# Kernel tuning notes

Hardware: AMD Instinct MI355X
Metric: run time of the kernel (lower is better)

## Reference

```python
import math
import jax, jax.numpy as jnp
import numpy as np

HEAD_DIM = 128
NUM_HEADS = 16
NUM_KV_HEADS = 4
CAUSAL = True


def rotate_half(x):
    x1 = x[..., : x.shape[-1] // 2]
    x2 = x[..., x.shape[-1] // 2 :]
    return jnp.concatenate([-x2, x1], axis=-1)


def setup_inputs() -> dict:
    key = jax.random.key(0)
    k1, k2, k3, k4, k5 = jax.random.split(key, 5)
    B, S, H = 2, 2048, 2048
    total_heads = NUM_HEADS + 2 * NUM_KV_HEADS  # 24
    hidden_states = jax.random.normal(k1, (B, S, H), dtype=jnp.float32)
    cos = jax.random.normal(k2, (S, HEAD_DIM), dtype=jnp.float32)
    sin = jax.random.normal(k3, (S, HEAD_DIM), dtype=jnp.float32)
    # eqx.nn.Linear weight layout: [out_features, in_features], y = W @ x
    w_qkv = jax.random.normal(k4, (total_heads * HEAD_DIM, H), dtype=jnp.float32) / math.sqrt(H)
    w_o = jax.random.normal(k5, (H, NUM_HEADS * HEAD_DIM), dtype=jnp.float32) / math.sqrt(NUM_HEADS * HEAD_DIM)
    return {"hidden_states": hidden_states, "cos": cos, "sin": sin, "w_qkv": w_qkv, "w_o": w_o}


def reference(hidden_states, cos, sin, w_qkv, w_o):
    B, S, _ = hidden_states.shape
    # fused QKV projection: [B,S,total_heads,head_dim]
    qkv = jnp.einsum("bsh,oh->bso", hidden_states, w_qkv).reshape(B, S, -1, HEAD_DIM)
    q = qkv[:, :, :NUM_HEADS]
    k = qkv[:, :, NUM_HEADS : NUM_HEADS + NUM_KV_HEADS]
    v = qkv[:, :, NUM_HEADS + NUM_KV_HEADS :]
    # RoPE: cos/sin [S,head_dim] -> broadcast [S,1,head_dim] over heads
    c = cos[..., None, :]
    s_ = sin[..., None, :]
    q = q * c + rotate_half(q) * s_
    k = k * c + rotate_half(k) * s_
    # GQA: repeat K/V across query-head groups
    rep = NUM_HEADS // NUM_KV_HEADS
    k = jnp.repeat(k, rep, axis=2)
    v = jnp.repeat(v, rep, axis=2)
    scale = 1.0 / math.sqrt(HEAD_DIM)
    scores = jnp.einsum("bshd,bthd->bhst", q, k) * scale  # [B,H,S,S]
    if CAUSAL:
        mask = jnp.tril(jnp.ones((S, S), dtype=bool))[None, None]
        scores = jnp.where(mask, scores, jnp.float32(-1e10))
    attn = jax.nn.softmax(scores, axis=-1)
    out = jnp.einsum("bhst,bthd->bshd", attn, v).reshape(B, S, -1)
    return jnp.einsum("bsd,od->bso", out, w_o)
```

## Files before the change

kernel.cpp:

```cpp
#include <hip/hip_runtime.h>
#include <hip/hip_bf16.h>
#include <stdint.h>

typedef __hip_bfloat16 bf16;
typedef __attribute__((ext_vector_type(8))) __bf16 bf16x8;
typedef __attribute__((ext_vector_type(4))) float f32x4;
typedef __attribute__((ext_vector_type(16))) float f32x16;
typedef __attribute__((ext_vector_type(4))) unsigned int u32x4;

#define QSCALE_LOG2E (0.08838834764831845f * 1.4426950408889634f)

__device__ __forceinline__ float fast_exp2(float x) {
#if __has_builtin(__builtin_amdgcn_exp2f)
  return __builtin_amdgcn_exp2f(x);
#else
  return exp2f(x);
#endif
}

__device__ __forceinline__ void gload_lds16(const void* g, void* l) {
  __builtin_amdgcn_global_load_lds(
      (__attribute__((address_space(1))) void*)(uintptr_t)g,
      (__attribute__((address_space(3))) void*)(uint32_t)(uintptr_t)l,
      16, 0, 0);
}

__global__ void cast_f32_to_bf16(const float* __restrict__ in,
                                 bf16* __restrict__ out, int n) {
  const int n4 = n >> 2;
  const int stride = gridDim.x * blockDim.x;
  for (int i = blockIdx.x * blockDim.x + threadIdx.x; i < n4; i += stride) {
    float4 v = reinterpret_cast<const float4*>(in)[i];
    bf16 tmp[4];
    tmp[0] = __float2bfloat16(v.x);
    tmp[1] = __float2bfloat16(v.y);
    tmp[2] = __float2bfloat16(v.z);
    tmp[3] = __float2bfloat16(v.w);
    reinterpret_cast<uint2*>(out)[i] = *reinterpret_cast<uint2*>(tmp);
  }
}

__device__ __forceinline__ void store_c(float v, bf16* p) { *p = __float2bfloat16(v); }
__device__ __forceinline__ void store_c(float v, float* p) { *p = v; }

__device__ __forceinline__ bf16x8 rd_swz(const bf16* base, int row, int ks, int hi) {
  const int byte = row * 128 + ((ks * 64 + hi * 16) ^ ((row & 7) << 4));
  return *reinterpret_cast<const bf16x8*>((const char*)base + byte);
}

__device__ __forceinline__ void stage_part(const bf16* __restrict__ g, int K,
                                           int kt, bf16* ldsBase, int part,
                                           int tid) {
  const int ga = part * 512 + tid;
  const int r = ga >> 3;
  const int gl = ga & 7;
  const int col = kt * 64 + ((gl ^ (r & 7)) << 3);
  gload_lds16(g + (size_t)r * K + col, (char*)ldsBase + ga * 16);
}

#define DS_A(QR)                                                              \
  _Pragma("unroll") for (int m = 0; m < 4; ++m)                               \
  _Pragma("unroll") for (int ks = 0; ks < 2; ++ks)                            \
      af[m][ks] = rd_swz(Acur, wm * 128 + (QR) * 64 + m * 16 + lr, ks, hi);

#define DS_B0()                                                               \
  _Pragma("unroll") for (int n = 0; n < NQ0; ++n)                             \
  _Pragma("unroll") for (int ks = 0; ks < 2; ++ks)                            \
      bf0[n][ks] = rd_swz(Bcur, wn * WN + n * 16 + lr, ks, hi);

#define DS_B1()                                                               \
  _Pragma("unroll") for (int n = 0; n < NQ1; ++n)                             \
  _Pragma("unroll") for (int ks = 0; ks < 2; ++ks)                            \
      bf1[n][ks] = rd_swz(Bcur, wn * WN + (NQ0 + n) * 16 + lr, ks, hi);

#define MFMA_Q0(QR)                                                           \
  __builtin_amdgcn_s_setprio(1);                                             \
  _Pragma("unroll") for (int ks = 0; ks < 2; ++ks)                            \
  _Pragma("unroll") for (int m = 0; m < 4; ++m)                               \
  _Pragma("unroll") for (int n = 0; n < NQ0; ++n)                             \
      acc[(QR) * 4 + m][n] = __builtin_amdgcn_mfma_f32_16x16x32_bf16(         \
          af[m][ks], bf0[n][ks], acc[(QR) * 4 + m][n], 0, 0, 0);              \
  __builtin_amdgcn_s_setprio(0);

#define MFMA_Q1(QR)                                                           \
  __builtin_amdgcn_s_setprio(1);                                             \
  _Pragma("unroll") for (int ks = 0; ks < 2; ++ks)                            \
  _Pragma("unroll") for (int m = 0; m < 4; ++m)                               \
  _Pragma("unroll") for (int n = 0; n < NQ1; ++n)                             \
      acc[(QR) * 4 + m][NQ0 + n] = __builtin_amdgcn_mfma_f32_16x16x32_bf16(   \
          af[m][ks], bf1[n][ks], acc[(QR) * 4 + m][NQ0 + n], 0, 0, 0);        \
  __builtin_amdgcn_s_setprio(0);

#define PHASE_SYNC_PRE()                                \
  __builtin_amdgcn_s_barrier();                         \
  asm volatile("s_waitcnt lgkmcnt(0)" ::: "memory");    \
  __builtin_amdgcn_sched_barrier(0);

#define PHASE_END() __builtin_amdgcn_s_barrier();

#define VMCNT_LB()                                                            \
  if constexpr (LB == 2) asm volatile("s_waitcnt vmcnt(2)" ::: "memory");     \
  else if constexpr (LB == 3) asm volatile("s_waitcnt vmcnt(3)" ::: "memory");\
  else asm volatile("s_waitcnt vmcnt(4)" ::: "memory");

template <int BN, typename OutT>
__global__ __launch_bounds__(512, 2) void gemm256(const bf16* __restrict__ A,
                                                  const bf16* __restrict__ B,
                                                  OutT* __restrict__ C,
                                                  int M, int N, int K, int NBX) {
  constexpr int NFRAG = BN / 64;
  constexpr int NQ0 = (NFRAG + 1) / 2;
  constexpr int NQ1 = NFRAG - NQ0;
  constexpr int WN = BN / 4;
  constexpr int LB = BN / 64;
  constexpr int LB0 = (LB + 1) / 2;
  constexpr int LB1 = LB - LB0;

  extern __shared__ bf16 sm[];
  bf16* A0 = sm;
  bf16* A1 = sm + 16384;
  bf16* B0 = sm + 32768;
  bf16* B1 = B0 + BN * 64;

  const int tid = threadIdx.x;
  const int lane = tid & 63;
  const int w = tid >> 6;
  const int wm = w >> 2;
  const int wn = w & 3;
  const int lr = lane & 15;
  const int hi = lane >> 4;

  const int nwg = gridDim.x;
  const int cpx = nwg >> 3;
  const int bid = blockIdx.x;
  const int wg = (bid & 7) * cpx + (bid >> 3);
  const int bx = wg % NBX;
  const int by = wg / NBX;
  const int row0 = by * 256;
  const int col0 = bx * BN;

  const bf16* Ag = A + (size_t)row0 * K;
  const bf16* Bg = B + (size_t)col0 * K;

#pragma unroll
  for (int p = 0; p < 4; ++p) stage_part(Ag, K, 0, A0, p, tid);
#pragma unroll
  for (int p = 0; p < LB; ++p) stage_part(Bg, K, 0, B0, p, tid);
#pragma unroll
  for (int p = 0; p < LB; ++p) stage_part(Bg, K, 1, B1, p, tid);
  VMCNT_LB();
  __builtin_amdgcn_s_barrier();

  f32x4 acc[8][NFRAG] = {};
  bf16x8 af[4][2], bf0[NQ0][2], bf1[NQ1 ? NQ1 : 1][2];

  const int iters = K >> 7;
  for (int i = 0; i < iters; ++i) {
    const bool g2 = (i + 1 < iters);
    const int t1 = 2 * i + 1, t2 = 2 * i + 2, t3 = 2 * i + 3;
    {
      const bf16* Acur = A0;
      const bf16* Bcur = B0;
      DS_A(0); DS_B0();
      stage_part(Ag, K, t1, A1, 0, tid);
      stage_part(Ag, K, t1, A1, 1, tid);
      PHASE_SYNC_PRE(); MFMA_Q0(0); PHASE_END();
      DS_B1();
      stage_part(Ag, K, t1, A1, 2, tid);
      stage_part(Ag, K, t1, A1, 3, tid);
      PHASE_SYNC_PRE(); MFMA_Q1(0); PHASE_END();
      DS_A(1);
      if (g2) {
#pragma unroll
        for (int p = 0; p < LB0; ++p) stage_part(Bg, K, t2, B0, p, tid);
      }
      PHASE_SYNC_PRE(); MFMA_Q0(1); PHASE_END();
      if (g2) {
#pragma unroll
        for (int p = 0; p < LB1; ++p) stage_part(Bg, K, t2, B0, LB0 + p, tid);
        VMCNT_LB();
      } else {
        asm volatile("s_waitcnt vmcnt(0)" ::: "memory");
      }
      PHASE_SYNC_PRE(); MFMA_Q1(1); PHASE_END();
    }
    {
      const bf16* Acur = A1;
      const bf16* Bcur = B1;
      DS_A(0); DS_B0();
      if (g2) {
        stage_part(Ag, K, t2, A0, 0, tid);
        stage_part(Ag, K, t2, A0, 1, tid);
      }
      PHASE_SYNC_PRE(); MFMA_Q0(0); PHASE_END();
      DS_B1();
      if (g2) {
        stage_part(Ag, K, t2, A0, 2, tid);
        stage_part(Ag, K, t2, A0, 3, tid);
      }
      PHASE_SYNC_PRE(); MFMA_Q1(0); PHASE_END();
      DS_A(1);
      if (g2) {
#pragma unroll
        for (int p = 0; p < LB0; ++p) stage_part(Bg, K, t3, B1, p, tid);
      }
      PHASE_SYNC_PRE(); MFMA_Q0(1); PHASE_END();
      if (g2) {
#pragma unroll
        for (int p = 0; p < LB1; ++p) stage_part(Bg, K, t3, B1, LB0 + p, tid);
        VMCNT_LB();
      } else {
        asm volatile("s_waitcnt vmcnt(0)" ::: "memory");
      }
      PHASE_SYNC_PRE(); MFMA_Q1(1); PHASE_END();
    }
  }

#pragma unroll
  for (int mi = 0; mi < 8; ++mi)
#pragma unroll
    for (int ni = 0; ni < NFRAG; ++ni)
#pragma unroll
      for (int j = 0; j < 4; ++j) {
        const int r = row0 + wm * 128 + mi * 16 + hi * 4 + j;
        const int cc = col0 + wn * WN + ni * 16 + lr;
        store_c(acc[mi][ni][j], &C[(size_t)r * N + cc]);
      }
}

__global__ void rope_scatter(const bf16* __restrict__ qkv,
                             const float* __restrict__ cs,
                             const float* __restrict__ sn,
                             bf16* __restrict__ Q, bf16* __restrict__ Kd) {
  const int tok = blockIdx.x;
  const int b = tok >> 11;
  const int s = tok & 2047;
  const bf16* row = qkv + (size_t)tok * 3072;
  for (int idx = threadIdx.x; idx < 1280; idx += blockDim.x) {
    const int head = idx >> 6;
    const int j = idx & 63;
    float x1 = __bfloat162float(row[head * 128 + j]);
    float x2 = __bfloat162float(row[head * 128 + j + 64]);
    const float c1 = cs[s * 128 + j];
    const float c2 = cs[s * 128 + j + 64];
    const float s1 = sn[s * 128 + j];
    const float s2 = sn[s * 128 + j + 64];
    float y1 = x1 * c1 - x2 * s1;
    float y2 = x2 * c2 + x1 * s2;
    bf16* dst;
    if (head < 16) {
      y1 *= QSCALE_LOG2E;
      y2 *= QSCALE_LOG2E;
      dst = Q + ((size_t)(b * 16 + head) * 2048 + s) * 128;
    } else {
      dst = Kd + ((size_t)(b * 4 + head - 16) * 2048 + s) * 128;
    }
    dst[j] = __float2bfloat16(y1);
    dst[j + 64] = __float2bfloat16(y2);
  }
}

__global__ __launch_bounds__(256) void vtrans(const bf16* __restrict__ qkv,
                                              bf16* __restrict__ Vt) {
  __shared__ bf16 tile[64 * 136];
  const int bid = blockIdx.x;
  const int stile = bid & 31;
  const int hv = (bid >> 5) & 3;
  const int b = bid >> 7;
  const int tid = threadIdx.x;
  const int tok0 = stile * 64;
  const bf16* src = qkv + (size_t)(b * 2048 + tok0) * 3072 + 2560 + hv * 128;
#pragma unroll
  for (int i = 0; i < 4; ++i) {
    const int c = tid + i * 256;
    const int r = c >> 4;
    const int off = (c & 15) * 8;
    uint4 d = *reinterpret_cast<const uint4*>(src + (size_t)r * 3072 + off);
    *reinterpret_cast<uint4*>(&tile[r * 136 + off]) = d;
  }
  __syncthreads();
  bf16* dst = Vt + ((size_t)(b * 4 + hv) * 128) * 2048 + tok0;
#pragma unroll
  for (int i = 0; i < 4; ++i) {
    const int o = tid + i * 256;
    const int d = o >> 3;
    const int s0 = (o & 7) * 8;
    bf16 vals[8];
#pragma unroll
    for (int j = 0; j < 8; ++j) vals[j] = tile[(s0 + j) * 136 + d];
    *reinterpret_cast<uint4*>(dst + (size_t)d * 2048 + s0) =
        *reinterpret_cast<const uint4*>(vals);
  }
}

__device__ __forceinline__ void stage_k(const bf16* __restrict__ Kb, int k0,
                                        bf16* dst, int w, int lane) {
#pragma unroll
  for (int i = 0; i < 4; ++i) {
    const int L16 = i * 256 + w * 64 + lane;
    const int row = L16 >> 4;
    const int colb = (L16 & 15) * 16;
    const int src = colb ^ ((row & 7) << 4);
    gload_lds16(Kb + (size_t)(k0 + row) * 128 + (src >> 1),
                (char*)dst + (i * 256 + w * 64) * 16);
  }
}

__device__ __forceinline__ void stage_v(const bf16* __restrict__ Vtb, int k0,
                                        bf16* dst, int w, int lane) {
#pragma unroll
  for (int i = 0; i < 4; ++i) {
    const int L16 = i * 256 + w * 64 + lane;
    const int row = L16 >> 3;
    const int colb = (L16 & 7) * 16;
    const int src = colb ^ ((row & 7) << 4);
    gload_lds16(Vtb + (size_t)row * 2048 + k0 + (src >> 1),
                (char*)dst + (i * 256 + w * 64) * 16);
  }
}

__device__ __forceinline__ bf16x8 lds_read_swz(const bf16* base, int row,
                                               int colElem, int rowBytes) {
  const int byte = row * rowBytes + (((colElem * 2) ^ ((row & 7) << 4)));
  return *reinterpret_cast<const bf16x8*>((const char*)base + byte);
}

__global__ __launch_bounds__(256, 2) void attn_fwd(const bf16* __restrict__ Qg,
                                                   const bf16* __restrict__ Kg,
                                                   const bf16* __restrict__ Vtg,
                                                   bf16* __restrict__ Og) {
  __shared__ bf16 Ks[2][64 * 128];
  __shared__ bf16 Vs[2][128 * 64];

  const int tid = threadIdx.x;
  const int lane = tid & 63;
  const int w = tid >> 6;
  const int bid = blockIdx.x;
  int qt, bh;
  if (bid < 256) { qt = bid & 15; bh = bid >> 4; }
  else           { qt = 15 - (bid & 15); bh = 16 + ((bid - 256) >> 4); }
  const int b = bh >> 4;
  const int h = bh & 15;
  const int kvh = h >> 2;
  const int q31 = lane & 31;
  const int hw = lane >> 5;

  const bf16* Qb = Qg + ((size_t)(b * 16 + h) * 2048) * 128;
  const bf16* Kb = Kg + ((size_t)(b * 4 + kvh) * 2048) * 128;
  const bf16* Vtb = Vtg + ((size_t)(b * 4 + kvh) * 128) * 2048;

  const int qw = qt * 128 + w * 32;

  bf16x8 qf[8];
#pragma unroll
  for (int db = 0; db < 8; ++db)
    qf[db] = *reinterpret_cast<const bf16x8*>(Qb + (size_t)(qw + q31) * 128 +
                                              db * 16 + hw * 8);

  f32x16 acc[4] = {};
  float mrow = -1e30f;
  float lsum = 0.f;

  const int nt = 2 * qt + 2;

  stage_k(Kb, 0, &Ks[0][0], w, lane);
  stage_v(Vtb, 0, &Vs[0][0], w, lane);

  for (int t = 0; t < nt; ++t) {
    const int cur = t & 1;
    if (t + 1 < nt) {
      stage_k(Kb, (t + 1) * 64, &Ks[cur ^ 1][0], w, lane);
      stage_v(Vtb, (t + 1) * 64, &Vs[cur ^ 1][0], w, lane);
      asm volatile("s_waitcnt vmcnt(8)" ::: "memory");
    } else {
      asm volatile("s_waitcnt vmcnt(0)" ::: "memory");
    }
    __builtin_amdgcn_s_barrier();
    __builtin_amdgcn_sched_barrier(0);

    const int k0 = t * 64;
    const bool active = (k0 <= qw + 31);
    if (active) {
      const bf16* Kt = &Ks[cur][0];
      const bf16* Vtl = &Vs[cur][0];

      f32x16 sacc[2] = {};
#pragma unroll
      for (int kb = 0; kb < 2; ++kb)
#pragma unroll
        for (int db = 0; db < 8; ++db) {
          bf16x8 kf = lds_read_swz(Kt, kb * 32 + q31, db * 16 + hw * 8, 256);
          sacc[kb] = __builtin_amdgcn_mfma_f32_32x32x16_bf16(kf, qf[db],
                                                             sacc[kb], 0, 0, 0);
        }

      float p[2][16];
#pragma unroll
      for (int kb = 0; kb < 2; ++kb)
#pragma unroll
        for (int r = 0; r < 16; ++r) p[kb][r] = sacc[kb][r];

      if (k0 + 63 > qw) {
        const int qg = qw + q31;
#pragma unroll
        for (int kb = 0; kb < 2; ++kb)
#pragma unroll
          for (int r = 0; r < 16; ++r) {
            const int k = k0 + kb * 32 + (r & 3) + 8 * (r >> 2) + 4 * hw;
            if (k > qg) p[kb][r] = -1e30f;
          }
      }

      float mt = p[0][0];
#pragma unroll
      for (int r = 1; r < 16; ++r) mt = fmaxf(mt, p[0][r]);
#pragma unroll
      for (int r = 0; r < 16; ++r) mt = fmaxf(mt, p[1][r]);
      mt = fmaxf(mt, __shfl_xor(mt, 32));

      if (__any(mt > mrow + 11.5f)) {
        const float mnew = fmaxf(mrow, mt);
        const float alpha = fast_exp2(mrow - mnew);
        mrow = mnew;
        lsum *= alpha;
        float areg[16];
#pragma unroll
        for (int r = 0; r < 16; ++r) {
          const int qloc = (r & 3) + 8 * (r >> 2) + 4 * hw;
          areg[r] = __shfl(alpha, qloc + (lane & 32));
        }
#pragma unroll
        for (int db = 0; db < 4; ++db)
#pragma unroll
          for (int r = 0; r < 16; ++r) acc[db][r] *= areg[r];
      }

      float rs = 0.f;
#pragma unroll
      for (int kb = 0; kb < 2; ++kb)
#pragma unroll
        for (int r = 0; r < 16; ++r) {
          const float pe = fast_exp2(p[kb][r] - mrow);
          p[kb][r] = pe;
          rs += pe;
        }
      rs += __shfl_xor(rs, 32);
      lsum += rs;

      unsigned int pk[2][8];
#pragma unroll
      for (int kb = 0; kb < 2; ++kb)
#pragma unroll
        for (int i = 0; i < 8; ++i)
          asm("v_cvt_pk_bf16_f32 %0, %1, %2"
              : "=v"(pk[kb][i])
              : "v"(p[kb][2 * i]), "v"(p[kb][2 * i + 1]));

#pragma unroll
      for (int kb16 = 0; kb16 < 4; ++kb16) {
        const int kb = kb16 >> 1;
        const int j0 = (kb16 & 1) * 4;
        unsigned int a0 = pk[kb][j0 + 0], b0 = pk[kb][j0 + 2];
        unsigned int a1 = pk[kb][j0 + 1], b1 = pk[kb][j0 + 3];
        asm volatile("v_permlane32_swap_b32 %0, %1" : "+v"(a0), "+v"(b0));
        asm volatile("v_permlane32_swap_b32 %0, %1" : "+v"(a1), "+v"(b1));
        u32x4 afu;
        afu.x = a0; afu.y = a1; afu.z = b0; afu.w = b1;
        bf16x8 pa;
        __builtin_memcpy(&pa, &afu, 16);
#pragma unroll
        for (int db = 0; db < 4; ++db) {
          bf16x8 vf = lds_read_swz(Vtl, db * 32 + q31, kb16 * 16 + hw * 8, 128);
          acc[db] = __builtin_amdgcn_mfma_f32_32x32x16_bf16(pa, vf,
                                                            acc[db], 0, 0, 0);
        }
      }
    }

    __builtin_amdgcn_sched_barrier(0);
    __builtin_amdgcn_s_barrier();
  }

  const float inv = 1.0f / lsum;
  float invq[16];
#pragma unroll
  for (int r = 0; r < 16; ++r) {
    const int qloc = (r & 3) + 8 * (r >> 2) + 4 * hw;
    invq[r] = __shfl(inv, qloc + (lane & 32));
  }
#pragma unroll
  for (int db = 0; db < 4; ++db)
#pragma unroll
    for (int r = 0; r < 16; ++r) {
      const int qg = qw + (r & 3) + 8 * (r >> 2) + 4 * hw;
      const int dg = db * 32 + q31;
      Og[((size_t)(b * 2048 + qg)) * 2048 + h * 128 + dg] =
          __float2bfloat16(acc[db][r] * invq[r]);
    }
}

extern "C" void kernel_launch(void* const* d_in, const int* in_sizes, int n_in,
                              void* d_out, int out_size, void* d_ws,
                              size_t ws_size, hipStream_t stream) {
  const float* hidden = (const float*)d_in[0];
  const float* cs = (const float*)d_in[1];
  const float* sn = (const float*)d_in[2];
  const float* wqkv = (const float*)d_in[3];
  const float* wo = (const float*)d_in[4];
  float* out = (float*)d_out;

  bf16* p = (bf16*)d_ws;
  bf16* hid_b = p;   p += 8388608;
  bf16* wqkv_b = p;  p += 6291456;
  bf16* wo_b = p;    p += 4194304;
  bf16* qkv = p;     p += 12582912;
  bf16* Qs = p;      p += 8388608;
  bf16* Ksc = p;     p += 2097152;
  bf16* Vt = p;      p += 2097152;

  (void)hipFuncSetAttribute((const void*)gemm256<192, bf16>,
                            hipFuncAttributeMaxDynamicSharedMemorySize, 131072);
  (void)hipFuncSetAttribute((const void*)gemm256<128, float>,
                            hipFuncAttributeMaxDynamicSharedMemorySize, 131072);

  cast_f32_to_bf16<<<2048, 256, 0, stream>>>(hidden, hid_b, 8388608);
  cast_f32_to_bf16<<<1536, 256, 0, stream>>>(wqkv, wqkv_b, 6291456);
  cast_f32_to_bf16<<<1024, 256, 0, stream>>>(wo, wo_b, 4194304);

  gemm256<192, bf16><<<256, 512, 114688, stream>>>(hid_b, wqkv_b, qkv,
                                                   4096, 3072, 2048, 16);
  rope_scatter<<<4096, 256, 0, stream>>>(qkv, cs, sn, Qs, Ksc);
  vtrans<<<256, 256, 0, stream>>>(qkv, Vt);

  bf16* aout = hid_b;
  attn_fwd<<<512, 256, 0, stream>>>(Qs, Ksc, Vt, aout);

  gemm256<128, float><<<256, 512, 98304, stream>>>(aout, wo_b, out,
                                                   4096, 2048, 2048, 16);
}
```

Baseline: 176.7 us.

## Fuse three cast kernels and prefetch V fragments with MFMA priority hints

Merges the three f32-to-bf16 cast launches into one grid-stride kernel, which removes two launches and the gaps between them. In the attention loop, all V fragments are now read from LDS into registers ahead of time, half before and half after the QK MFMAs. This lets LDS latency overlap with matrix work. s_setprio is raised around the MFMA blocks to favour issuing them across waves. The cost is 16 extra bf16x8 registers per thread, which may reduce occupancy or cause spills.

```diff
diff --git a/kernel.cpp b/kernel.cpp
--- a/kernel.cpp
+++ b/kernel.cpp
@@ -25,18 +25,25 @@
       16, 0, 0);
 }
 
-__global__ void cast_f32_to_bf16(const float* __restrict__ in,
-                                 bf16* __restrict__ out, int n) {
-  const int n4 = n >> 2;
+__global__ void cast3(const float* __restrict__ h, const float* __restrict__ wq,
+                      const float* __restrict__ wo, bf16* __restrict__ oh,
+                      bf16* __restrict__ owq, bf16* __restrict__ owo) {
+  const int total = 4718592;
   const int stride = gridDim.x * blockDim.x;
-  for (int i = blockIdx.x * blockDim.x + threadIdx.x; i < n4; i += stride) {
-    float4 v = reinterpret_cast<const float4*>(in)[i];
+  for (int c = blockIdx.x * blockDim.x + threadIdx.x; c < total; c += stride) {
+    const float* src;
+    bf16* dst;
+    int i;
+    if (c < 2097152) { src = h; dst = oh; i = c; }
+    else if (c < 3670016) { src = wq; dst = owq; i = c - 2097152; }
+    else { src = wo; dst = owo; i = c - 3670016; }
+    float4 v = reinterpret_cast<const float4*>(src)[i];
     bf16 tmp[4];
     tmp[0] = __float2bfloat16(v.x);
     tmp[1] = __float2bfloat16(v.y);
     tmp[2] = __float2bfloat16(v.z);
     tmp[3] = __float2bfloat16(v.w);
-    reinterpret_cast<uint2*>(out)[i] = *reinterpret_cast<uint2*>(tmp);
+    reinterpret_cast<uint2*>(dst)[i] = *reinterpret_cast<uint2*>(tmp);
   }
 }
 
@@ -384,7 +391,15 @@
       const bf16* Kt = &Ks[cur][0];
       const bf16* Vtl = &Vs[cur][0];
 
+      bf16x8 va[8];
+#pragma unroll
+      for (int i = 0; i < 8; ++i) {
+        const int kb16 = i >> 2, db = i & 3;
+        va[i] = lds_read_swz(Vtl, db * 32 + q31, kb16 * 16 + hw * 8, 128);
+      }
+
       f32x16 sacc[2] = {};
+      __builtin_amdgcn_s_setprio(1);
 #pragma unroll
       for (int kb = 0; kb < 2; ++kb)
 #pragma unroll
@@ -393,6 +408,14 @@
           sacc[kb] = __builtin_amdgcn_mfma_f32_32x32x16_bf16(kf, qf[db],
                                                              sacc[kb], 0, 0, 0);
         }
+      __builtin_amdgcn_s_setprio(0);
+
+      bf16x8 vb[8];
+#pragma unroll
+      for (int i = 0; i < 8; ++i) {
+        const int kb16 = 2 + (i >> 2), db = i & 3;
+        vb[i] = lds_read_swz(Vtl, db * 32 + q31, kb16 * 16 + hw * 8, 128);
+      }
 
       float p[2][16];
 #pragma unroll
@@ -468,12 +491,14 @@
         afu.x = a0; afu.y = a1; afu.z = b0; afu.w = b1;
         bf16x8 pa;
         __builtin_memcpy(&pa, &afu, 16);
+        __builtin_amdgcn_s_setprio(1);
 #pragma unroll
         for (int db = 0; db < 4; ++db) {
-          bf16x8 vf = lds_read_swz(Vtl, db * 32 + q31, kb16 * 16 + hw * 8, 128);
+          const bf16x8 vf = (kb16 < 2) ? va[kb16 * 4 + db] : vb[(kb16 - 2) * 4 + db];
           acc[db] = __builtin_amdgcn_mfma_f32_32x32x16_bf16(pa, vf,
                                                             acc[db], 0, 0, 0);
         }
+        __builtin_amdgcn_s_setprio(0);
       }
     }
 
@@ -523,9 +548,7 @@
   (void)hipFuncSetAttribute((const void*)gemm256<128, float>,
                             hipFuncAttributeMaxDynamicSharedMemorySize, 131072);
 
-  cast_f32_to_bf16<<<2048, 256, 0, stream>>>(hidden, hid_b, 8388608);
-  cast_f32_to_bf16<<<1536, 256, 0, stream>>>(wqkv, wqkv_b, 6291456);
-  cast_f32_to_bf16<<<1024, 256, 0, stream>>>(wo, wo_b, 4194304);
+  cast3<<<2048, 256, 0, stream>>>(hidden, wqkv, wo, hid_b, wqkv_b, wo_b);
 
   gemm256<192, bf16><<<256, 512, 114688, stream>>>(hid_b, wqkv_b, qkv,
                                                    4096, 3072, 2048, 16);
```

New measurement: 174.8 us. No clear change (-1.1%).
